# Performance work log

Hardware: AMD Instinct MI355X
Metric: run time of the kernel (lower is better)

## Reference

```python
import jax, jax.numpy as jnp
import numpy as np

N = 50000
E = 800000
IN_DIM = 128
HID = 64
HEADS = 4

def _gat_layer(h, src, dst, W, al, ar, Wres, activation):
    # h: [N, F_in]; W: [F_in, HEADS*HID]; al/ar: [HEADS, HID]
    n = h.shape[0]
    ft = (h @ W).reshape(n, HEADS, HID)                    # [N,H,D]
    el = (ft * al).sum(-1)                                  # [N,H]
    er = (ft * ar).sum(-1)                                  # [N,H]
    e = jax.nn.leaky_relu(el[src] + er[dst], 0.2)           # [E,H]
    m = jax.ops.segment_max(e, dst, num_segments=n)         # per-dst max for stable softmax
    ex = jnp.exp(e - m[dst])
    den = jax.ops.segment_sum(ex, dst, num_segments=n)
    alpha = ex / den[dst]                                   # edge softmax [E,H]
    out = jax.ops.segment_sum(alpha[:, :, None] * ft[src], dst, num_segments=n)  # [N,H,D]
    res = (h @ Wres).reshape(n, HEADS, HID) if Wres is not None else h.reshape(n, HEADS, HID)
    out = out + res
    return activation(out) if activation is not None else out


def setup_inputs() -> dict:
    key = jax.random.key(0)
    ks = jax.random.split(key, 16)
    def lin(k, fi, fo):
        return jax.random.normal(k, (fi, fo), jnp.float32) / np.sqrt(fi)
    HD = HEADS * HID
    inp = {
        "h": jax.random.normal(ks[0], (N, IN_DIM), jnp.float32),
        "src": jax.random.randint(ks[1], (E,), 0, N, jnp.int32),
        "dst": jax.random.randint(ks[2], (E,), 0, N, jnp.int32),
        "W1": lin(ks[3], IN_DIM, HD),
        "Wr1": lin(ks[4], IN_DIM, HD),
        "al1": jax.random.normal(ks[5], (HEADS, HID), jnp.float32) * 0.1,
        "ar1": jax.random.normal(ks[6], (HEADS, HID), jnp.float32) * 0.1,
        "W2": lin(ks[7], HD, HD),
        "al2": jax.random.normal(ks[8], (HEADS, HID), jnp.float32) * 0.1,
        "ar2": jax.random.normal(ks[9], (HEADS, HID), jnp.float32) * 0.1,
        "W3": lin(ks[10], HD, HD),
        "al3": jax.random.normal(ks[11], (HEADS, HID), jnp.float32) * 0.1,
        "ar3": jax.random.normal(ks[12], (HEADS, HID), jnp.float32) * 0.1,
        "Wm1": lin(ks[13], HID, HID),
        "bm1": jnp.zeros((HID,), jnp.float32),
        "Wm2": lin(ks[14], HID, 1),
        "bm2": jnp.zeros((1,), jnp.float32),
    }
    return inp


def reference(h, src, dst, W1, Wr1, al1, ar1, W2, al2, ar2, W3, al3, ar3, Wm1, bm1, Wm2, bm2):
    x = _gat_layer(h, src, dst, W1, al1, ar1, Wr1, jax.nn.relu)   # [N,H,D]
    x = x.reshape(x.shape[0], -1)                                  # [N,H*D]
    x = _gat_layer(x, src, dst, W2, al2, ar2, None, jax.nn.relu)  # identity residual (in==H*D)
    x = x.reshape(x.shape[0], -1)
    x = _gat_layer(x, src, dst, W3, al3, ar3, None, None)
    hf = x.mean(1)                                                 # [N,HID]
    diff = jnp.abs(hf[src] - hf[dst])                              # [E,HID]
    z = jax.nn.relu(diff @ Wm1 + bm1)
    score = jax.nn.sigmoid(z @ Wm2 + bm2).squeeze(-1)              # [E]
    return score
```

## Files before the change

### kernel.cpp

```cpp
#include <hip/hip_runtime.h>
#include <hip/hip_bf16.h>

typedef unsigned short u16;
typedef unsigned char u8;
typedef __attribute__((ext_vector_type(8))) short bf16x8;
typedef __attribute__((ext_vector_type(4))) float f32x4;
typedef __attribute__((ext_vector_type(2))) float f32x2;

__device__ __forceinline__ float bf2f(u16 u){
  union { unsigned int i; float f; } v; v.i = ((unsigned int)u) << 16; return v.f;
}
__device__ __forceinline__ u16 f2bf(float f){
  union { float f; unsigned int i; } v; v.f = f;
  unsigned int lsb = (v.i >> 16) & 1u;
  v.i += 0x7fffu + lsb;
  return (u16)(v.i >> 16);
}
__device__ __forceinline__ unsigned pkbf(float a, float b){
  __hip_bfloat162 h = __float22bfloat162_rn(make_float2(a, b));
  union { __hip_bfloat162 h2; unsigned u; } c; c.h2 = h; return c.u;
}
__device__ __forceinline__ u8 f2fp8(float f){
  int p = __builtin_amdgcn_cvt_pk_fp8_f32(f, f, 0, false);
  return (u8)(p & 0xFF);
}

__global__ void k_sniff(const u16* __restrict__ p, int* __restrict__ flag){
  __shared__ int s[256];
  int tid = threadIdx.x;
  u16 v = p[2 * tid];
  int e = (v >> 7) & 0xFF;
  s[tid] = (e >= 100 && e <= 135) ? 1 : 0;
  __syncthreads();
  for (int off = 128; off; off >>= 1){
    if (tid < off) s[tid] += s[tid + off];
    __syncthreads();
  }
  if (tid == 0) *flag = (s[0] < 180) ? 1 : 0;
}

__global__ __launch_bounds__(1024) void k_csrpos(const int* __restrict__ dst,
                                                 int* __restrict__ slot,
                                                 int* __restrict__ cnt, int N, int E){
  __shared__ int bins[1024];
  const int nblk = gridDim.x;
  const int R = (N + nblk - 1) / nblk;
  const int lo = blockIdx.x * R;
  const int hi = min(lo + R, N);
  const int nb = hi - lo;
  for (int i = threadIdx.x; i < nb; i += 1024) bins[i] = 0;
  __syncthreads();
  const int E4 = E >> 2;
  for (int i = threadIdx.x; i < E4; i += 1024){
    int4 d4 = ((const int4*)dst)[i];
    int e = i << 2;
    int x;
    x = d4.x - lo; if ((unsigned)x < (unsigned)nb) slot[e]     = atomicAdd(&bins[x], 1);
    x = d4.y - lo; if ((unsigned)x < (unsigned)nb) slot[e + 1] = atomicAdd(&bins[x], 1);
    x = d4.z - lo; if ((unsigned)x < (unsigned)nb) slot[e + 2] = atomicAdd(&bins[x], 1);
    x = d4.w - lo; if ((unsigned)x < (unsigned)nb) slot[e + 3] = atomicAdd(&bins[x], 1);
  }
  for (int e = (E4 << 2) + threadIdx.x; e < E; e += 1024){
    int x = dst[e] - lo;
    if ((unsigned)x < (unsigned)nb) slot[e] = atomicAdd(&bins[x], 1);
  }
  __syncthreads();
  for (int i = threadIdx.x; i < nb; i += 1024) cnt[lo + i] = bins[i];
}

struct PrepEnt { const void* s; void* d; void* d2; int n; int K; int mode; int bstart; };
struct Prep16 { PrepEnt e[16]; };
__global__ void k_prep(Prep16 tab, const u16* __restrict__ hsrc){
  __shared__ int s[256];
  __shared__ u16 tl[32][33];
  {
    int tid = threadIdx.x;
    u16 v = hsrc[2 * tid];
    int e = (v >> 7) & 0xFF;
    s[tid] = (e >= 100 && e <= 135) ? 1 : 0;
    __syncthreads();
    for (int off = 128; off; off >>= 1){
      if (tid < off) s[tid] += s[tid + off];
      __syncthreads();
    }
  }
  const int flag = (s[0] < 180) ? 1 : 0;
  __syncthreads();

  const int bx = blockIdx.x;
  int y = 0;
  #pragma unroll
  for (int i = 1; i < 16; ++i) if (bx >= tab.e[i].bstart) y = i;
  PrepEnt en = tab.e[y];
  const int nblk = ((y < 15) ? tab.e[y + 1].bstart : (int)gridDim.x) - en.bstart;
  const int lb = bx - en.bstart;
  const int T = nblk * 256;
  const int t0 = lb * 256 + threadIdx.x;

  if (en.mode == 1){
    u16* d = (u16*)en.d;
    for (int i = t0; i < en.n; i += T){
      u16 o[4];
      if (flag){
        float4 v = ((const float4*)en.s)[i];
        o[0] = f2bf(v.x); o[1] = f2bf(v.y); o[2] = f2bf(v.z); o[3] = f2bf(v.w);
      } else {
        uint2 v = ((const uint2*)en.s)[i];
        o[0] = (u16)v.x; o[1] = (u16)(v.x >> 16); o[2] = (u16)v.y; o[3] = (u16)(v.y >> 16);
      }
      uint2 w; w.x = o[0] | ((unsigned)o[1] << 16); w.y = o[2] | ((unsigned)o[3] << 16);
      ((uint2*)d)[i] = w;
    }
  } else if (en.mode == 0){
    u16* d = (u16*)en.d;
    for (int i = t0; i < en.n; i += T){
      if (flag) d[i] = f2bf(((const float*)en.s)[i]);
      else      d[i] = ((const u16*)en.s)[i];
    }
  } else if (en.mode == 2){
    u16* wt = (u16*)en.d;
    const int K = en.K;
    const int tk = lb >> 3, tc = lb & 7;
    const int tx = threadIdx.x & 31, ty = threadIdx.x >> 5;
    #pragma unroll
    for (int r = 0; r < 4; ++r){
      int row = tk * 32 + ty + r * 8, col = tc * 32 + tx;
      u16 b;
      if (flag) b = f2bf(((const float*)en.s)[row * 256 + col]);
      else      b = ((const u16*)en.s)[row * 256 + col];
      tl[ty + r * 8][tx] = b;
    }
    __syncthreads();
    #pragma unroll
    for (int r = 0; r < 4; ++r){
      int c = tc * 32 + ty + r * 8, k = tk * 32 + tx;
      wt[(size_t)c * K + k] = tl[tx][ty + r * 8];
    }
  }
}

__global__ void k_scan1(const int* __restrict__ cnt, int* __restrict__ rowptr,
                        int* __restrict__ bsums, int N){
  __shared__ int s[256];
  int i = blockIdx.x * 256 + threadIdx.x;
  int v = (i < N) ? cnt[i] : 0;
  s[threadIdx.x] = v; __syncthreads();
  for (int off = 1; off < 256; off <<= 1){
    int x = 0;
    if (threadIdx.x >= off) x = s[threadIdx.x - off];
    __syncthreads();
    s[threadIdx.x] += x;
    __syncthreads();
  }
  if (i < N) rowptr[i + 1] = s[threadIdx.x];
  if (threadIdx.x == 255) bsums[blockIdx.x] = s[255];
}
__global__ void k_scan2(int* __restrict__ bsums, int nb){
  __shared__ int s[256];
  int t = threadIdx.x;
  int v = (t < nb) ? bsums[t] : 0;
  s[t] = v; __syncthreads();
  for (int off = 1; off < 256; off <<= 1){
    int x = 0;
    if (t >= off) x = s[t - off];
    __syncthreads();
    s[t] += x;
    __syncthreads();
  }
  if (t < nb) bsums[t] = s[t] - v;
}
__global__ void k_scan3(int* __restrict__ rowptr, const int* __restrict__ bsums, int N){
  int i = blockIdx.x * 256 + threadIdx.x;
  if (i < N){
    rowptr[i + 1] += bsums[blockIdx.x];
    if (i == 0) rowptr[0] = 0;
  }
}
__global__ void k_place(const int* __restrict__ src, const int* __restrict__ dst,
                        const int* __restrict__ slot, const int* __restrict__ rowptr,
                        int4* __restrict__ csrp, int E){
  const int T = gridDim.x * 256;
  for (int i = blockIdx.x * 256 + threadIdx.x; i < E; i += T){
    int d = dst[i];
    csrp[rowptr[d] + slot[i]] = make_int4(src[i], d, i, 0);
  }
}
__global__ void k_extract(const int4* __restrict__ csrp, int* __restrict__ csrs, int E){
  int i = blockIdx.x * 256 + threadIdx.x;
  if (i < E) csrs[i] = csrp[i].x;
}

#define GWAIT6() asm volatile("s_waitcnt vmcnt(6)" ::: "memory")
#define GWAIT0() asm volatile("s_waitcnt vmcnt(0)" ::: "memory")
#define GBAR()   do { __builtin_amdgcn_s_barrier(); __builtin_amdgcn_sched_barrier(0); } while (0)

__global__ __launch_bounds__(256, 5) void mfma_gemm_v7(
    const u16* __restrict__ X, const u16* __restrict__ WT, const u16* __restrict__ WTr,
    u8* __restrict__ FT8, u16* __restrict__ XA,
    const u16* __restrict__ al, const u16* __restrict__ ar,
    float* __restrict__ el4, float* __restrict__ er4, int N, int K)
{
  extern __shared__ u16 Bs[];
  const int wv = threadIdx.x >> 6;
  const int lane = threadIdx.x & 63;
  const int m = lane & 15;
  const int q = lane >> 4;
  const int mh = m & 7;
  const int row0 = blockIdx.x * 64 + wv * 16;
  const int col0 = blockIdx.y * 128;
  const u16* W = (blockIdx.z == 0) ? WT : WTr;

  f32x4 acc[8];
  #pragma unroll
  for (int t = 0; t < 8; ++t) acc[t] = (f32x4){0.f, 0.f, 0.f, 0.f};
  const int rA = row0 + m;
  const bool vA = rA < N;
  const u16* apA = X + (size_t)rA * K + q * 8;

  auto stageC = [&](int c, int buf){
    u16* base = Bs + buf * 8192;
    const u16* Wk = W + c * 64;
    #pragma unroll
    for (int j = 0; j < 4; ++j){
      int cbase = (j * 4 + wv) * 64;
      int ci = cbase + lane;
      int col = ci >> 3, slot = ci & 7;
      int gslot = slot ^ (col & 7);
      const u16* srcp = Wk + (size_t)(col0 + col) * K + gslot * 8;
      __builtin_amdgcn_global_load_lds((const unsigned int*)srcp,
                                       (unsigned int*)(base + cbase * 8), 16, 0, 0);
    }
  };
  auto loadA = [&](int c, bf16x8* a){
    const int kb = c * 64;
    bf16x8 z = {};
    a[0] = z; a[1] = z;
    if (vA){ a[0] = *(const bf16x8*)(apA + kb); a[1] = *(const bf16x8*)(apA + kb + 32); }
  };
  auto compute = [&](const u16* __restrict__ Bb, const bf16x8* a){
    #pragma unroll
    for (int ks = 0; ks < 2; ++ks){
      const int sb = ks * 4 + q;
      #pragma unroll
      for (int t = 0; t < 8; ++t){
        const u16* bp = Bb + (size_t)(t * 16 + m) * 64 + (size_t)(sb ^ mh) * 8;
        bf16x8 b = *(const bf16x8*)bp;
        acc[t] = __builtin_amdgcn_mfma_f32_16x16x32_bf16(b, a[ks], acc[t], 0, 0, 0);
      }
    }
  };

  const int nc = K >> 6;
  bf16x8 a0[2], a1[2];
  stageC(0, 0);
  loadA(0, a0);
  for (int c = 0; c < nc; c += 2){
    if (c + 1 < nc){ stageC(c + 1, 1); loadA(c + 1, a1); GWAIT6(); }
    else           { GWAIT0(); }
    GBAR();
    compute(Bs, a0);
    GBAR();
    if (c + 1 < nc){
      if (c + 2 < nc){ stageC(c + 2, 0); loadA(c + 2, a0); GWAIT6(); }
      else           { GWAIT0(); }
      GBAR();
      compute(Bs + 8192, a1);
      GBAR();
    }
  }

  if (blockIdx.z == 0){
    uint2 alp[8], arp[8];
    #pragma unroll
    for (int t = 0; t < 8; ++t){
      alp[t] = *(const uint2*)(al + col0 + t * 16 + q * 4);
      arp[t] = *(const uint2*)(ar + col0 + t * 16 + q * 4);
    }
    auto halv = [](uint2 p, int r) -> float {
      unsigned w = (r < 2) ? p.x : p.y;
      return bf2f((u16)((r & 1) ? (w >> 16) : (w & 0xffff)));
    };
    float pe[2] = {0.f, 0.f}, pr[2] = {0.f, 0.f};
    #pragma unroll
    for (int t = 0; t < 8; ++t)
      #pragma unroll
      for (int r = 0; r < 4; ++r){
        pe[t >> 2] += acc[t][r] * halv(alp[t], r);
        pr[t >> 2] += acc[t][r] * halv(arp[t], r);
      }
    pe[0] += __shfl_xor(pe[0], 16); pe[0] += __shfl_xor(pe[0], 32);
    pe[1] += __shfl_xor(pe[1], 16); pe[1] += __shfl_xor(pe[1], 32);
    pr[0] += __shfl_xor(pr[0], 16); pr[0] += __shfl_xor(pr[0], 32);
    pr[1] += __shfl_xor(pr[1], 16); pr[1] += __shfl_xor(pr[1], 32);
    if (q == 0 && vA){
      *(float2*)(el4 + (size_t)rA * 4 + blockIdx.y * 2) = make_float2(pe[0], pe[1]);
      *(float2*)(er4 + (size_t)rA * 4 + blockIdx.y * 2) = make_float2(pr[0], pr[1]);
    }
    if (vA){
      u8* op = FT8 + (size_t)rA * 256 + col0 + q * 4;
      #pragma unroll
      for (int t = 0; t < 8; ++t){
        int pw = __builtin_amdgcn_cvt_pk_fp8_f32(acc[t][0], acc[t][1], 0, false);
        pw = __builtin_amdgcn_cvt_pk_fp8_f32(acc[t][2], acc[t][3], pw, true);
        *(int*)(op + t * 16) = pw;
      }
    }
  } else {
    if (vA){
      u16* op = XA + (size_t)rA * 256 + col0 + q * 4;
      #pragma unroll
      for (int t = 0; t < 8; ++t){
        uint2 w;
        w.x = pkbf(acc[t][0], acc[t][1]);
        w.y = pkbf(acc[t][2], acc[t][3]);
        *(uint2*)(op + t * 16) = w;
      }
    }
  }
}

__global__ __launch_bounds__(256) void aggregate8(
    const u8* __restrict__ ft8, const float* __restrict__ el4, const float* __restrict__ er4,
    const int* __restrict__ rowptr, const int* __restrict__ csrs,
    const u16* __restrict__ residb, u16* __restrict__ outb,
    u16* __restrict__ hf, int do_hf, int N)
{
  __shared__ float sal[4][4][17][4];
  __shared__ int   sof[4][4][16];
  const int w = threadIdx.x >> 6, lane = threadIdx.x & 63;
  const int g = lane >> 4, t = lane & 15;
  const int hd = t >> 2;
  const int d = blockIdx.x * 16 + w * 4 + g;
  const bool vd = d < N;
  int beg = 0, deg = 0;
  if (vd){ beg = rowptr[d]; deg = rowptr[d + 1] - beg; }
  int mdeg = deg;
  mdeg = max(mdeg, __shfl_xor(mdeg, 16));
  mdeg = max(mdeg, __shfl_xor(mdeg, 32));
  float4 erd = make_float4(0.f, 0.f, 0.f, 0.f);
  if (vd) erd = ((const float4*)er4)[d];

  f32x2 acc2[8];
  #pragma unroll
  for (int i = 0; i < 8; ++i) acc2[i] = (f32x2){0.f, 0.f};
  float den[4] = {0.f, 0.f, 0.f, 0.f};

  for (int c0 = 0; c0 < mdeg; c0 += 16){
    const int rem = deg - c0;
    float t0 = 0.f, t1 = 0.f, t2 = 0.f, t3 = 0.f; int s = 0;
    if (t < rem){
      s = csrs[beg + c0 + t];
      float4 ql = ((const float4*)el4)[s];
      float e0 = ql.x + erd.x; e0 = (e0 > 0.f) ? e0 : 0.2f * e0;
      float e1 = ql.y + erd.y; e1 = (e1 > 0.f) ? e1 : 0.2f * e1;
      float e2 = ql.z + erd.z; e2 = (e2 > 0.f) ? e2 : 0.2f * e2;
      float e3 = ql.w + erd.w; e3 = (e3 > 0.f) ? e3 : 0.2f * e3;
      t0 = __expf(fminf(e0, 60.f)); t1 = __expf(fminf(e1, 60.f));
      t2 = __expf(fminf(e2, 60.f)); t3 = __expf(fminf(e3, 60.f));
    }
    den[0] += t0; den[1] += t1; den[2] += t2; den[3] += t3;
    sal[w][g][t][0] = t0; sal[w][g][t][1] = t1;
    sal[w][g][t][2] = t2; sal[w][g][t][3] = t3;
    sof[w][g][t] = s << 8;
    __builtin_amdgcn_wave_barrier();
    int cr = rem < 16 ? (rem < 0 ? 0 : rem) : 16;
    int jm = (cr + 3) & ~3;
    for (int j = 0; j < jm; j += 4){
      float a[4]; unsigned off[4]; uint4 v[4];
      #pragma unroll
      for (int u = 0; u < 4; ++u){
        a[u] = sal[w][g][j + u][hd];
        off[u] = (unsigned)sof[w][g][j + u];
      }
      #pragma unroll
      for (int u = 0; u < 4; ++u)
        v[u] = *(const uint4*)(ft8 + (size_t)off[u] + t * 16);
      #pragma unroll
      for (int u = 0; u < 4; ++u){
        f32x2 a2 = (f32x2){a[u], a[u]};
        acc2[0] += __builtin_amdgcn_cvt_pk_f32_fp8(v[u].x, 0) * a2;
        acc2[1] += __builtin_amdgcn_cvt_pk_f32_fp8(v[u].x, 1) * a2;
        acc2[2] += __builtin_amdgcn_cvt_pk_f32_fp8(v[u].y, 0) * a2;
        acc2[3] += __builtin_amdgcn_cvt_pk_f32_fp8(v[u].y, 1) * a2;
        acc2[4] += __builtin_amdgcn_cvt_pk_f32_fp8(v[u].z, 0) * a2;
        acc2[5] += __builtin_amdgcn_cvt_pk_f32_fp8(v[u].z, 1) * a2;
        acc2[6] += __builtin_amdgcn_cvt_pk_f32_fp8(v[u].w, 0) * a2;
        acc2[7] += __builtin_amdgcn_cvt_pk_f32_fp8(v[u].w, 1) * a2;
      }
    }
    __builtin_amdgcn_wave_barrier();
  }
  #pragma unroll
  for (int mk = 1; mk < 16; mk <<= 1){
    den[0] += __shfl_xor(den[0], mk); den[1] += __shfl_xor(den[1], mk);
    den[2] += __shfl_xor(den[2], mk); den[3] += __shfl_xor(den[3], mk);
  }
  const float dh = den[hd];
  const float inv = (dh > 0.f) ? (1.f / dh) : 0.f;

  if (!vd) return;
  const u16* rp = residb + (size_t)d * 256 + t * 16;
  uint4 r0 = *(const uint4*)rp;
  uint4 r1 = *(const uint4*)(rp + 8);
  float o[16];
  {
    union { unsigned u; float f; } x;
    unsigned rw[8] = {r0.x, r0.y, r0.z, r0.w, r1.x, r1.y, r1.z, r1.w};
    #pragma unroll
    for (int i = 0; i < 8; ++i){
      x.u = rw[i] << 16;          o[2 * i]     = x.f;
      x.u = rw[i] & 0xffff0000u;  o[2 * i + 1] = x.f;
    }
  }
  #pragma unroll
  for (int i = 0; i < 8; ++i){
    o[2 * i]     += acc2[i].x * inv;
    o[2 * i + 1] += acc2[i].y * inv;
  }
  if (!do_hf){
    uint4 a, b;
    a.x = pkbf(fmaxf(o[0], 0.f),  fmaxf(o[1], 0.f));
    a.y = pkbf(fmaxf(o[2], 0.f),  fmaxf(o[3], 0.f));
    a.z = pkbf(fmaxf(o[4], 0.f),  fmaxf(o[5], 0.f));
    a.w = pkbf(fmaxf(o[6], 0.f),  fmaxf(o[7], 0.f));
    b.x = pkbf(fmaxf(o[8], 0.f),  fmaxf(o[9], 0.f));
    b.y = pkbf(fmaxf(o[10], 0.f), fmaxf(o[11], 0.f));
    b.z = pkbf(fmaxf(o[12], 0.f), fmaxf(o[13], 0.f));
    b.w = pkbf(fmaxf(o[14], 0.f), fmaxf(o[15], 0.f));
    u16* op = outb + (size_t)d * 256 + t * 16;
    *(uint4*)op = a;
    *(uint4*)(op + 8) = b;
  } else {
    #pragma unroll
    for (int i = 0; i < 16; ++i){
      float v = o[i];
      v += __shfl_xor(v, 4);
      v += __shfl_xor(v, 8);
      o[i] = 0.25f * v;
    }
    if (t < 4){
      uint4 a, b;
      a.x = pkbf(o[0], o[1]);   a.y = pkbf(o[2], o[3]);
      a.z = pkbf(o[4], o[5]);   a.w = pkbf(o[6], o[7]);
      b.x = pkbf(o[8], o[9]);   b.y = pkbf(o[10], o[11]);
      b.z = pkbf(o[12], o[13]); b.w = pkbf(o[14], o[15]);
      u16* hp = hf + (size_t)d * 64 + t * 16;
      *(uint4*)hp = a;
      *(uint4*)(hp + 8) = b;
    }
  }
}

__global__ __launch_bounds__(256) void edge_mlp_csr(
    const u16* __restrict__ hfb, const int4* __restrict__ csrp,
    const u16* __restrict__ Wm1, const u16* __restrict__ bm1,
    const u16* __restrict__ Wm2, const u16* __restrict__ bm2,
    void* __restrict__ out, int E, const int* __restrict__ flag)
{
  const int lane = threadIdx.x & 63;
  const int m = lane & 15;
  const int q = lane >> 4;
  const int is_f32 = *flag;

  bf16x8 bfr[4][2];
  #pragma unroll
  for (int t = 0; t < 4; ++t)
    #pragma unroll
    for (int ks = 0; ks < 2; ++ks)
      #pragma unroll
      for (int j = 0; j < 8; ++j)
        bfr[t][ks][j] = (short)Wm1[(size_t)(ks * 32 + q * 8 + j) * 64 + t * 16 + m];

  float b1v[4], w2v[4];
  #pragma unroll
  for (int t = 0; t < 4; ++t){
    b1v[t] = bf2f(bm1[t * 16 + m]);
    w2v[t] = bf2f(Wm2[t * 16 + m]);
  }
  const float b2 = bf2f(bm2[0]);

  const int wid = blockIdx.x * 4 + (threadIdx.x >> 6);
  const int nw  = gridDim.x * 4;
  for (int e0 = wid * 16; e0 < E; e0 += nw * 16){
    int e = e0 + m; if (e >= E) e = E - 1;
    int4 ed = csrp[e];
    const u16* ps = hfb + (size_t)ed.x * 64;
    const u16* pd = hfb + (size_t)ed.y * 64;
    union { bf16x8 v; uint4 u; } af[2];
    #pragma unroll
    for (int ks = 0; ks < 2; ++ks){
      bf16x8 vs = *(const bf16x8*)(ps + ks * 32 + q * 8);
      bf16x8 vd = *(const bf16x8*)(pd + ks * 32 + q * 8);
      unsigned pk[4];
      #pragma unroll
      for (int pp = 0; pp < 4; ++pp){
        float a0 = fabsf(bf2f((u16)vs[2 * pp])     - bf2f((u16)vd[2 * pp]));
        float a1 = fabsf(bf2f((u16)vs[2 * pp + 1]) - bf2f((u16)vd[2 * pp + 1]));
        pk[pp] = pkbf(a0, a1);
      }
      af[ks].u = make_uint4(pk[0], pk[1], pk[2], pk[3]);
    }
    f32x4 acc[4];
    #pragma unroll
    for (int t = 0; t < 4; ++t) acc[t] = (f32x4){0.f, 0.f, 0.f, 0.f};
    #pragma unroll
    for (int ks = 0; ks < 2; ++ks)
      #pragma unroll
      for (int t = 0; t < 4; ++t)
        acc[t] = __builtin_amdgcn_mfma_f32_16x16x32_bf16(af[ks].v, bfr[t][ks], acc[t], 0, 0, 0);
    #pragma unroll
    for (int r = 0; r < 4; ++r){
      float p = 0.f;
      #pragma unroll
      for (int t = 0; t < 4; ++t)
        p += fmaxf(acc[t][r] + b1v[t], 0.f) * w2v[t];
      #pragma unroll
      for (int mm = 1; mm < 16; mm <<= 1) p += __shfl_xor(p, mm);
      int slot = e0 + q * 4 + r;
      if (m == 0 && slot < E){
        int eid = csrp[slot].z;
        float sc = 1.f / (1.f + __expf(-(p + b2)));
        if (is_f32) ((float*)out)[eid] = sc;
        else        ((u16*)out)[eid]   = f2bf(sc);
      }
    }
  }
}

extern "C" void kernel_launch(void* const* d_in, const int* in_sizes, int n_in,
                              void* d_out, int out_size, void* d_ws, size_t ws_size,
                              hipStream_t stream)
{
  const int* src = (const int*)d_in[1];
  const int* dst = (const int*)d_in[2];

  const int N = in_sizes[0] / 128;
  const int E = in_sizes[1];

  char* p = (char*)d_ws;
  auto alloc = [&](size_t bytes) -> char* {
    char* r = p; p += (bytes + 255) & ~(size_t)255; return r;
  };
  int* flag   = (int*)  alloc(4);
  u16* hc     = (u16*)  alloc((size_t)N * 128 * 2);
  u8*  FT8    = (u8*)   alloc((size_t)N * 256);
  u16* XA     = (u16*)  alloc((size_t)N * 256 * 2);
  u16* XB     = (u16*)  alloc((size_t)N * 256 * 2);
  float* el   = (float*)alloc((size_t)N * 4 * 4);
  float* er   = (float*)alloc((size_t)N * 4 * 4);
  u16* hfb    = (u16*)  alloc((size_t)N * 64 * 2);
  int* rowptr = (int*)  alloc((size_t)(N + 1) * 4);
  int* cnt    = (int*)  alloc((size_t)N * 4);
  int* slot   = (int*)  alloc((size_t)E * 4);
  int4* csrp  = (int4*) alloc((size_t)E * 16);
  int* csrs   = (int*)  alloc((size_t)E * 4);
  int* bsums  = (int*)  alloc(1024);
  u16* WT1    = (u16*)  alloc(128 * 256 * 2);
  u16* WTr1   = (u16*)  alloc(128 * 256 * 2);
  u16* WT2    = (u16*)  alloc(256 * 256 * 2);
  u16* WT3    = (u16*)  alloc(256 * 256 * 2);
  u16* al1c   = (u16*)  alloc(256 * 2);
  u16* ar1c   = (u16*)  alloc(256 * 2);
  u16* al2c   = (u16*)  alloc(256 * 2);
  u16* ar2c   = (u16*)  alloc(256 * 2);
  u16* al3c   = (u16*)  alloc(256 * 2);
  u16* ar3c   = (u16*)  alloc(256 * 2);
  u16* Wm1c   = (u16*)  alloc(4096 * 2);
  u16* bm1c   = (u16*)  alloc(64 * 2);
  u16* Wm2c   = (u16*)  alloc(64 * 2);
  u16* bm2c   = (u16*)  alloc(2);

  const int nb = (N + 255) / 256;
  const int ge = (E + 255) / 256;
  const u16* hsrc = (const u16*)d_in[0];

  k_sniff<<<1, 256, 0, stream>>>(hsrc, flag);

  {
    int nbp = (N + 1023) / 1024;
    if (nbp < 64) nbp = 64;
    k_csrpos<<<nbp, 1024, 0, stream>>>(dst, slot, cnt, N, E);
  }

  {
    Prep16 t{};
    int b = 0;
    auto put = [&](int idx, const void* s, void* d, void* d2, int n, int K,
                   int mode, int nblk){
      t.e[idx] = {s, d, d2, n, K, mode, b};
      b += nblk;
    };
    put(0,  d_in[0],  hc,    nullptr, N * 32,   0,   1, 768);
    put(1,  d_in[3],  WT1,   nullptr, 0,        128, 2, 32);
    put(2,  d_in[4],  WTr1,  nullptr, 0,        128, 2, 32);
    put(3,  d_in[7],  WT2,   nullptr, 0,        256, 2, 64);
    put(4,  d_in[10], WT3,   nullptr, 0,        256, 2, 64);
    put(5,  d_in[5],  al1c,  nullptr, 256,      0,   0, 1);
    put(6,  d_in[6],  ar1c,  nullptr, 256,      0,   0, 1);
    put(7,  d_in[8],  al2c,  nullptr, 256,      0,   0, 1);
    put(8,  d_in[9],  ar2c,  nullptr, 256,      0,   0, 1);
    put(9,  d_in[11], al3c,  nullptr, 256,      0,   0, 1);
    put(10, d_in[12], ar3c,  nullptr, 256,      0,   0, 1);
    put(11, d_in[13], Wm1c,  nullptr, 4096,     0,   0, 1);
    put(12, d_in[14], bm1c,  nullptr, 64,       0,   0, 1);
    put(13, d_in[15], Wm2c,  nullptr, 64,       0,   0, 1);
    put(14, d_in[16], bm2c,  nullptr, 1,        0,   0, 1);
    put(15, nullptr,  nullptr, nullptr, 0,      0,   0, 0);
    k_prep<<<dim3(b), 256, 0, stream>>>(t, hsrc);
  }

  k_scan1<<<nb, 256, 0, stream>>>(cnt, rowptr, bsums, N);
  k_scan2<<<1, 256, 0, stream>>>(bsums, nb);
  k_scan3<<<nb, 256, 0, stream>>>(rowptr, bsums, N);
  k_place<<<512, 256, 0, stream>>>(src, dst, slot, rowptr, csrp, E);
  k_extract<<<ge, 256, 0, stream>>>(csrp, csrs, E);

  const dim3 gA3((N + 63) / 64, 2);
  const dim3 gL1((N + 63) / 64, 2, 2);
  const int gG = (N + 15) / 16;
  const int ldsP = 2 * 128 * 64 * 2;

  mfma_gemm_v7<<<gL1, 256, ldsP, stream>>>(hc, WT1, WTr1, FT8, XA, al1c, ar1c,
                                           el, er, N, 128);
  aggregate8<<<gG, 256, 0, stream>>>(FT8, el, er, rowptr, csrs, XA, XB, nullptr, 0, N);
  mfma_gemm_v7<<<gA3, 256, ldsP, stream>>>(XB, WT2, WT2, FT8, XA, al2c, ar2c,
                                           el, er, N, 256);
  aggregate8<<<gG, 256, 0, stream>>>(FT8, el, er, rowptr, csrs, XB, XA, nullptr, 0, N);
  mfma_gemm_v7<<<gA3, 256, ldsP, stream>>>(XA, WT3, WT3, FT8, XB, al3c, ar3c,
                                           el, er, N, 256);
  aggregate8<<<gG, 256, 0, stream>>>(FT8, el, er, rowptr, csrs, XA, nullptr, hfb, 1, N);
  edge_mlp_csr<<<2048, 256, 0, stream>>>(hfb, csrp, Wm1c, bm1c, Wm2c, bm2c,
                                         d_out, E, flag);
}
```

Measured before the change: 459.7 us.

## Make GEMM persistent with resident weights and fuse CSR slotting into layer-1 GEMM

The GEMM kernel now loads the full weight slab into LDS once per block and loops persistently over row tiles, prefetching the next A tile into registers. This replaces the per-K-chunk double-buffered staging and barriers. The separate k_csrpos kernel is removed. Its per-edge slot counting moves into the tail of the layer-1 GEMM using global atomics on a zeroed counter array, saving a launch. Global atomics may contend more than the old LDS binning, and the larger LDS footprint lowers occupancy.

```diff
diff --git a/kernel.cpp b/kernel.cpp
--- a/kernel.cpp
+++ b/kernel.cpp
@@ -37,35 +37,6 @@
     __syncthreads();
   }
   if (tid == 0) *flag = (s[0] < 180) ? 1 : 0;
-}
-
-__global__ __launch_bounds__(1024) void k_csrpos(const int* __restrict__ dst,
-                                                 int* __restrict__ slot,
-                                                 int* __restrict__ cnt, int N, int E){
-  __shared__ int bins[1024];
-  const int nblk = gridDim.x;
-  const int R = (N + nblk - 1) / nblk;
-  const int lo = blockIdx.x * R;
-  const int hi = min(lo + R, N);
-  const int nb = hi - lo;
-  for (int i = threadIdx.x; i < nb; i += 1024) bins[i] = 0;
-  __syncthreads();
-  const int E4 = E >> 2;
-  for (int i = threadIdx.x; i < E4; i += 1024){
-    int4 d4 = ((const int4*)dst)[i];
-    int e = i << 2;
-    int x;
-    x = d4.x - lo; if ((unsigned)x < (unsigned)nb) slot[e]     = atomicAdd(&bins[x], 1);
-    x = d4.y - lo; if ((unsigned)x < (unsigned)nb) slot[e + 1] = atomicAdd(&bins[x], 1);
-    x = d4.z - lo; if ((unsigned)x < (unsigned)nb) slot[e + 2] = atomicAdd(&bins[x], 1);
-    x = d4.w - lo; if ((unsigned)x < (unsigned)nb) slot[e + 3] = atomicAdd(&bins[x], 1);
-  }
-  for (int e = (E4 << 2) + threadIdx.x; e < E; e += 1024){
-    int x = dst[e] - lo;
-    if ((unsigned)x < (unsigned)nb) slot[e] = atomicAdd(&bins[x], 1);
-  }
-  __syncthreads();
-  for (int i = threadIdx.x; i < nb; i += 1024) cnt[lo + i] = bins[i];
 }
 
 struct PrepEnt { const void* s; void* d; void* d2; int n; int K; int mode; int bstart; };
@@ -190,131 +161,158 @@
   if (i < E) csrs[i] = csrp[i].x;
 }
 
-#define GWAIT6() asm volatile("s_waitcnt vmcnt(6)" ::: "memory")
-#define GWAIT0() asm volatile("s_waitcnt vmcnt(0)" ::: "memory")
-#define GBAR()   do { __builtin_amdgcn_s_barrier(); __builtin_amdgcn_sched_barrier(0); } while (0)
-
-__global__ __launch_bounds__(256, 5) void mfma_gemm_v7(
+template<int K, int L1>
+__global__ __launch_bounds__(256, (K == 128) ? 4 : 2) void mfma_gemm_v8(
     const u16* __restrict__ X, const u16* __restrict__ WT, const u16* __restrict__ WTr,
     u8* __restrict__ FT8, u16* __restrict__ XA,
     const u16* __restrict__ al, const u16* __restrict__ ar,
-    float* __restrict__ el4, float* __restrict__ er4, int N, int K)
+    float* __restrict__ el4, float* __restrict__ er4, int N,
+    const int* __restrict__ edst, int* __restrict__ slotp, int* __restrict__ cur,
+    int Etot)
 {
+  constexpr int NF = K / 32;
+  constexpr int SPR = K / 8;
+  constexpr int ISH = (SPR == 32) ? 5 : 4;
   extern __shared__ u16 Bs[];
   const int wv = threadIdx.x >> 6;
   const int lane = threadIdx.x & 63;
   const int m = lane & 15;
   const int q = lane >> 4;
   const int mh = m & 7;
-  const int row0 = blockIdx.x * 64 + wv * 16;
-  const int col0 = blockIdx.y * 128;
-  const u16* W = (blockIdx.z == 0) ? WT : WTr;
-
-  f32x4 acc[8];
+  int colsel, zsel;
+  if (L1){ colsel = blockIdx.x & 1; zsel = blockIdx.x >> 1; }
+  else   { colsel = blockIdx.x;     zsel = 0; }
+  const int col0 = colsel * 128;
+  const u16* W = (zsel == 0) ? WT : WTr;
+
   #pragma unroll
-  for (int t = 0; t < 8; ++t) acc[t] = (f32x4){0.f, 0.f, 0.f, 0.f};
-  const int rA = row0 + m;
-  const bool vA = rA < N;
-  const u16* apA = X + (size_t)rA * K + q * 8;
-
-  auto stageC = [&](int c, int buf){
-    u16* base = Bs + buf * 8192;
-    const u16* Wk = W + c * 64;
-    #pragma unroll
-    for (int j = 0; j < 4; ++j){
-      int cbase = (j * 4 + wv) * 64;
-      int ci = cbase + lane;
-      int col = ci >> 3, slot = ci & 7;
-      int gslot = slot ^ (col & 7);
-      const u16* srcp = Wk + (size_t)(col0 + col) * K + gslot * 8;
-      __builtin_amdgcn_global_load_lds((const unsigned int*)srcp,
-                                       (unsigned int*)(base + cbase * 8), 16, 0, 0);
+  for (int j = 0; j < K / 16; ++j){
+    int cbase = (j * 4 + wv) * 64;
+    int chunk = cbase + lane;
+    int col = chunk >> ISH;
+    int slot = chunk & (SPR - 1);
+    int gslot = slot ^ (col & 7);
+    const u16* srcp = W + (size_t)(col0 + col) * K + gslot * 8;
+    __builtin_amdgcn_global_load_lds((const unsigned int*)srcp,
+                                     (unsigned int*)(Bs + cbase * 8), 16, 0, 0);
+  }
+
+  const int RT = (N + 63) >> 6;
+  const int G = gridDim.y;
+  int rt = blockIdx.y;
+
+  bf16x8 aC[NF], aN[NF];
+  auto loadA = [&](int rtile, bf16x8* a){
+    int r = rtile * 64 + wv * 16 + m;
+    bf16x8 z = {};
+    #pragma unroll
+    for (int f = 0; f < NF; ++f) a[f] = z;
+    if (r < N){
+      const u16* ap = X + (size_t)r * K + q * 8;
+      #pragma unroll
+      for (int f = 0; f < NF; ++f) a[f] = *(const bf16x8*)(ap + f * 32);
     }
   };
-  auto loadA = [&](int c, bf16x8* a){
-    const int kb = c * 64;
-    bf16x8 z = {};
-    a[0] = z; a[1] = z;
-    if (vA){ a[0] = *(const bf16x8*)(apA + kb); a[1] = *(const bf16x8*)(apA + kb + 32); }
-  };
-  auto compute = [&](const u16* __restrict__ Bb, const bf16x8* a){
-    #pragma unroll
-    for (int ks = 0; ks < 2; ++ks){
-      const int sb = ks * 4 + q;
-      #pragma unroll
-      for (int t = 0; t < 8; ++t){
-        const u16* bp = Bb + (size_t)(t * 16 + m) * 64 + (size_t)(sb ^ mh) * 8;
-        bf16x8 b = *(const bf16x8*)bp;
-        acc[t] = __builtin_amdgcn_mfma_f32_16x16x32_bf16(b, a[ks], acc[t], 0, 0, 0);
-      }
-    }
-  };
-
-  const int nc = K >> 6;
-  bf16x8 a0[2], a1[2];
-  stageC(0, 0);
-  loadA(0, a0);
-  for (int c = 0; c < nc; c += 2){
-    if (c + 1 < nc){ stageC(c + 1, 1); loadA(c + 1, a1); GWAIT6(); }
-    else           { GWAIT0(); }
-    GBAR();
-    compute(Bs, a0);
-    GBAR();
-    if (c + 1 < nc){
-      if (c + 2 < nc){ stageC(c + 2, 0); loadA(c + 2, a0); GWAIT6(); }
-      else           { GWAIT0(); }
-      GBAR();
-      compute(Bs + 8192, a1);
-      GBAR();
-    }
-  }
-
-  if (blockIdx.z == 0){
-    uint2 alp[8], arp[8];
+
+  uint2 alp[8], arp[8];
+  if (zsel == 0){
     #pragma unroll
     for (int t = 0; t < 8; ++t){
       alp[t] = *(const uint2*)(al + col0 + t * 16 + q * 4);
       arp[t] = *(const uint2*)(ar + col0 + t * 16 + q * 4);
     }
-    auto halv = [](uint2 p, int r) -> float {
-      unsigned w = (r < 2) ? p.x : p.y;
-      return bf2f((u16)((r & 1) ? (w >> 16) : (w & 0xffff)));
-    };
-    float pe[2] = {0.f, 0.f}, pr[2] = {0.f, 0.f};
-    #pragma unroll
-    for (int t = 0; t < 8; ++t)
-      #pragma unroll
-      for (int r = 0; r < 4; ++r){
-        pe[t >> 2] += acc[t][r] * halv(alp[t], r);
-        pr[t >> 2] += acc[t][r] * halv(arp[t], r);
-      }
-    pe[0] += __shfl_xor(pe[0], 16); pe[0] += __shfl_xor(pe[0], 32);
-    pe[1] += __shfl_xor(pe[1], 16); pe[1] += __shfl_xor(pe[1], 32);
-    pr[0] += __shfl_xor(pr[0], 16); pr[0] += __shfl_xor(pr[0], 32);
-    pr[1] += __shfl_xor(pr[1], 16); pr[1] += __shfl_xor(pr[1], 32);
-    if (q == 0 && vA){
-      *(float2*)(el4 + (size_t)rA * 4 + blockIdx.y * 2) = make_float2(pe[0], pe[1]);
-      *(float2*)(er4 + (size_t)rA * 4 + blockIdx.y * 2) = make_float2(pr[0], pr[1]);
-    }
-    if (vA){
-      u8* op = FT8 + (size_t)rA * 256 + col0 + q * 4;
+  }
+  auto halv = [](uint2 p, int r) -> float {
+    unsigned w = (r < 2) ? p.x : p.y;
+    return bf2f((u16)((r & 1) ? (w >> 16) : (w & 0xffff)));
+  };
+
+  if (rt < RT) loadA(rt, aC);
+  asm volatile("s_waitcnt vmcnt(0)" ::: "memory");
+  __syncthreads();
+
+  for (; rt < RT; rt += G){
+    if (rt + G < RT) loadA(rt + G, aN);
+    f32x4 acc[8];
+    #pragma unroll
+    for (int t = 0; t < 8; ++t) acc[t] = (f32x4){0.f, 0.f, 0.f, 0.f};
+    #pragma unroll
+    for (int ks = 0; ks < NF; ++ks){
+      const int sb = ks * 4 + q;
       #pragma unroll
       for (int t = 0; t < 8; ++t){
-        int pw = __builtin_amdgcn_cvt_pk_fp8_f32(acc[t][0], acc[t][1], 0, false);
-        pw = __builtin_amdgcn_cvt_pk_fp8_f32(acc[t][2], acc[t][3], pw, true);
-        *(int*)(op + t * 16) = pw;
-      }
-    }
-  } else {
-    if (vA){
-      u16* op = XA + (size_t)rA * 256 + col0 + q * 4;
-      #pragma unroll
-      for (int t = 0; t < 8; ++t){
-        uint2 w;
-        w.x = pkbf(acc[t][0], acc[t][1]);
-        w.y = pkbf(acc[t][2], acc[t][3]);
-        *(uint2*)(op + t * 16) = w;
-      }
+        const u16* bp = Bs + (size_t)(t * 16 + m) * K + (size_t)(sb ^ mh) * 8;
+        bf16x8 b = *(const bf16x8*)bp;
+        acc[t] = __builtin_amdgcn_mfma_f32_16x16x32_bf16(b, aC[ks], acc[t], 0, 0, 0);
+      }
+    }
+    const int rA = rt * 64 + wv * 16 + m;
+    const bool vA = rA < N;
+    if (zsel == 0){
+      float pe[2] = {0.f, 0.f}, pr[2] = {0.f, 0.f};
+      #pragma unroll
+      for (int t = 0; t < 8; ++t)
+        #pragma unroll
+        for (int r = 0; r < 4; ++r){
+          pe[t >> 2] += acc[t][r] * halv(alp[t], r);
+          pr[t >> 2] += acc[t][r] * halv(arp[t], r);
+        }
+      pe[0] += __shfl_xor(pe[0], 16); pe[0] += __shfl_xor(pe[0], 32);
+      pe[1] += __shfl_xor(pe[1], 16); pe[1] += __shfl_xor(pe[1], 32);
+      pr[0] += __shfl_xor(pr[0], 16); pr[0] += __shfl_xor(pr[0], 32);
+      pr[1] += __shfl_xor(pr[1], 16); pr[1] += __shfl_xor(pr[1], 32);
+      if (q == 0 && vA){
+        *(float2*)(el4 + (size_t)rA * 4 + colsel * 2) = make_float2(pe[0], pe[1]);
+        *(float2*)(er4 + (size_t)rA * 4 + colsel * 2) = make_float2(pr[0], pr[1]);
+      }
+      if (vA){
+        u8* op = FT8 + (size_t)rA * 256 + col0 + q * 4;
+        #pragma unroll
+        for (int t = 0; t < 8; ++t){
+          int pw = __builtin_amdgcn_cvt_pk_fp8_f32(acc[t][0], acc[t][1], 0, false);
+          pw = __builtin_amdgcn_cvt_pk_fp8_f32(acc[t][2], acc[t][3], pw, true);
+          *(int*)(op + t * 16) = pw;
+        }
+      }
+    } else {
+      if (vA){
+        u16* op = XA + (size_t)rA * 256 + col0 + q * 4;
+        #pragma unroll
+        for (int t = 0; t < 8; ++t){
+          uint2 w;
+          w.x = pkbf(acc[t][0], acc[t][1]);
+          w.y = pkbf(acc[t][2], acc[t][3]);
+          *(uint2*)(op + t * 16) = w;
+        }
+      }
+    }
+    #pragma unroll
+    for (int f = 0; f < NF; ++f) aC[f] = aN[f];
+  }
+
+  if (L1){
+    const int nbk = (int)(gridDim.x * gridDim.y);
+    const int bid = (int)(blockIdx.y * gridDim.x + blockIdx.x);
+    const int epb = (Etot + nbk - 1) / nbk;
+    const int elo = bid * epb;
+    const int ehi = min(elo + epb, Etot);
+    const int tid = (int)threadIdx.x;
+    int e0 = elo + tid, e1 = e0 + 256, e2 = e0 + 512;
+    bool b0 = e0 < ehi, b1 = e1 < ehi, b2 = e2 < ehi;
+    int d0 = 0, d1 = 0, d2 = 0;
+    if (b0) d0 = edst[e0];
+    if (b1) d1 = edst[e1];
+    if (b2) d2 = edst[e2];
+    int p0 = 0, p1 = 0, p2 = 0;
+    if (b0) p0 = atomicAdd(&cur[d0], 1);
+    if (b1) p1 = atomicAdd(&cur[d1], 1);
+    if (b2) p2 = atomicAdd(&cur[d2], 1);
+    if (b0) slotp[e0] = p0;
+    if (b1) slotp[e1] = p1;
+    if (b2) slotp[e2] = p2;
+    for (int e = elo + tid + 768; e < ehi; e += 256){
+      int dd = edst[e];
+      slotp[e] = atomicAdd(&cur[dd], 1);
     }
   }
 }
@@ -550,7 +548,7 @@
   float* er   = (float*)alloc((size_t)N * 4 * 4);
   u16* hfb    = (u16*)  alloc((size_t)N * 64 * 2);
   int* rowptr = (int*)  alloc((size_t)(N + 1) * 4);
-  int* cnt    = (int*)  alloc((size_t)N * 4);
+  int* cur    = (int*)  alloc((size_t)N * 4);
   int* slot   = (int*)  alloc((size_t)E * 4);
   int4* csrp  = (int4*) alloc((size_t)E * 16);
   int* csrs   = (int*)  alloc((size_t)E * 4);
@@ -575,12 +573,7 @@
   const u16* hsrc = (const u16*)d_in[0];
 
   k_sniff<<<1, 256, 0, stream>>>(hsrc, flag);
-
-  {
-    int nbp = (N + 1023) / 1024;
-    if (nbp < 64) nbp = 64;
-    k_csrpos<<<nbp, 1024, 0, stream>>>(dst, slot, cnt, N, E);
-  }
+  hipMemsetAsync(cur, 0, (size_t)N * 4, stream);
 
   {
     Prep16 t{};
@@ -609,25 +602,24 @@
     k_prep<<<dim3(b), 256, 0, stream>>>(t, hsrc);
   }
 
-  k_scan1<<<nb, 256, 0, stream>>>(cnt, rowptr, bsums, N);
+  const int gG = (N + 15) / 16;
+  const int lds1 = 128 * 128 * 2;
+  const int lds2 = 128 * 256 * 2;
+
+  mfma_gemm_v8<128, 1><<<dim3(4, 256), 256, lds1, stream>>>(
+      hc, WT1, WTr1, FT8, XA, al1c, ar1c, el, er, N, dst, slot, cur, E);
+  k_scan1<<<nb, 256, 0, stream>>>(cur, rowptr, bsums, N);
   k_scan2<<<1, 256, 0, stream>>>(bsums, nb);
   k_scan3<<<nb, 256, 0, stream>>>(rowptr, bsums, N);
   k_place<<<512, 256, 0, stream>>>(src, dst, slot, rowptr, csrp, E);
   k_extract<<<ge, 256, 0, stream>>>(csrp, csrs, E);
 
-  const dim3 gA3((N + 63) / 64, 2);
-  const dim3 gL1((N + 63) / 64, 2, 2);
-  const int gG = (N + 15) / 16;
-  const int ldsP = 2 * 128 * 64 * 2;
-
-  mfma_gemm_v7<<<gL1, 256, ldsP, stream>>>(hc, WT1, WTr1, FT8, XA, al1c, ar1c,
-                                           el, er, N, 128);
   aggregate8<<<gG, 256, 0, stream>>>(FT8, el, er, rowptr, csrs, XA, XB, nullptr, 0, N);
-  mfma_gemm_v7<<<gA3, 256, ldsP, stream>>>(XB, WT2, WT2, FT8, XA, al2c, ar2c,
-                                           el, er, N, 256);
+  mfma_gemm_v8<256, 0><<<dim3(2, 256), 256, lds2, stream>>>(
+      XB, WT2, WT2, FT8, XA, al2c, ar2c, el, er, N, nullptr, nullptr, nullptr, 0);
   aggregate8<<<gG, 256, 0, stream>>>(FT8, el, er, rowptr, csrs, XB, XA, nullptr, 0, N);
-  mfma_gemm_v7<<<gA3, 256, ldsP, stream>>>(XA, WT3, WT3, FT8, XB, al3c, ar3c,
-                                           el, er, N, 256);
+  mfma_gemm_v8<256, 0><<<dim3(2, 256), 256, lds2, stream>>>(
+      XA, WT3, WT3, FT8, XB, al3c, ar3c, el, er, N, nullptr, nullptr, nullptr, 0);
   aggregate8<<<gG, 256, 0, stream>>>(FT8, el, er, rowptr, csrs, XA, nullptr, hfb, 1, N);
   edge_mlp_csr<<<2048, 256, 0, stream>>>(hfb, csrp, Wm1c, bm1c, Wm2c, bm2c,
                                          d_out, E, flag);
```

Measured after the change: 605.5 us. 31.7% more time.
